# Optimization experiments

Hardware: AMD Instinct MI355X
Metric: run time of the kernel (lower is better)

Reference implementation:

```python
import jax, jax.numpy as jnp
import numpy as np

B, T, IN, H, OUT = 4096, 7, 512, 1024, 512


def setup_inputs() -> dict:
    key = jax.random.key(0)
    ks = jax.random.split(key, 13)
    s = 0.05  # weight init scale to keep gates/tanh unsaturated
    return {
        "x": jax.random.normal(ks[0], (B, T, IN), jnp.float32),
        "W_ih1": jax.random.normal(ks[1], (3 * H, IN), jnp.float32) * s,
        "W_hh1": jax.random.normal(ks[2], (3 * H, H), jnp.float32) * s,
        "b_ih1": jax.random.normal(ks[3], (3 * H,), jnp.float32) * s,
        "b_hh1": jax.random.normal(ks[4], (3 * H,), jnp.float32) * s,
        "W_ih2": jax.random.normal(ks[5], (3 * H, H), jnp.float32) * s,
        "W_hh2": jax.random.normal(ks[6], (3 * H, H), jnp.float32) * s,
        "b_ih2": jax.random.normal(ks[7], (3 * H,), jnp.float32) * s,
        "b_hh2": jax.random.normal(ks[8], (3 * H,), jnp.float32) * s,
        "Wo1": jax.random.normal(ks[9], (OUT, H), jnp.float32) * s,
        "bo1": jax.random.normal(ks[10], (OUT,), jnp.float32) * s,
        "Wo2": jax.random.normal(ks[11], (OUT, H), jnp.float32) * s,
        "bo2": jax.random.normal(ks[12], (OUT,), jnp.float32) * s,
    }


def gru_cell(x, h, W_ih, W_hh, b_ih, b_hh):
    # torch.nn.GRUCell math, gate order (r, z, n)
    gi = x @ W_ih.T + b_ih          # [B, 3H]
    gh = h @ W_hh.T + b_hh          # [B, 3H]
    i_r, i_z, i_n = jnp.split(gi, 3, axis=-1)
    h_r, h_z, h_n = jnp.split(gh, 3, axis=-1)
    r = jax.nn.sigmoid(i_r + h_r)
    z = jax.nn.sigmoid(i_z + h_z)
    n = jnp.tanh(i_n + r * h_n)
    return (1.0 - z) * n + z * h


def reference(x, W_ih1, W_hh1, b_ih1, b_hh1, W_ih2, W_hh2, b_ih2, b_hh2,
              Wo1, bo1, Wo2, bo2):
    batch = x.shape[0]
    h1_0 = jnp.zeros((batch, H), x.dtype)
    h2_0 = jnp.zeros((batch, H), x.dtype)

    def step(carry, x_t):
        h1, h2 = carry
        h1 = gru_cell(x_t, h1, W_ih1, W_hh1, b_ih1, b_hh1)
        h2 = gru_cell(h1, h2, W_ih2, W_hh2, b_ih2, b_hh2)
        out = jnp.tanh(h1 @ Wo1.T + bo1) + jnp.tanh(h2 @ Wo2.T + bo2)
        # s_t_cached starts as T zeros and only T steps run, so the popped
        # cached state is always zeros: mse(h2, 0) == mean(h2**2)
        aux = jnp.mean(jnp.square(h2))
        return (h1, h2), (out, aux)

    xs = jnp.swapaxes(x, 0, 1)  # [T, B, IN]
    _, (outs, auxs) = jax.lax.scan(step, (h1_0, h2_0), xs)
    outputs = jnp.swapaxes(outs, 0, 1)  # [B, T, OUT]
    aux_loss = jnp.sum(auxs)
    return outputs, aux_loss
```

## Files before the change

kernel.cpp:

```cpp
#include <hip/hip_runtime.h>
#include <cstdint>

#define BB   4096
#define TT   7
#define INF  512
#define HH   1024
#define OUTF 512
#define G3   3072

typedef short bf16x8 __attribute__((ext_vector_type(8)));
typedef float f32x4  __attribute__((ext_vector_type(4)));

static __device__ __forceinline__ unsigned short f2bf(float f) {
  unsigned u = __float_as_uint(f);
  unsigned r = ((u >> 16) & 1u) + 0x7FFFu;
  return (unsigned short)((u + r) >> 16);
}
static __device__ __forceinline__ float bf2f(unsigned short s) {
  return __uint_as_float(((unsigned)s) << 16);
}

#define GLDS16(gp, lp)                                                        \
  __builtin_amdgcn_global_load_lds(                                           \
      (const __attribute__((address_space(1))) void*)(gp),                    \
      (__attribute__((address_space(3))) void*)(lp), 16, 0, 0)

__device__ __forceinline__ int xcd_swz(int bid, int nwg) {
  return (bid & 7) * (nwg >> 3) + (bid >> 3);
}

__global__ __launch_bounds__(256)
void cvt_f32_to_bf16_x4(const float* __restrict__ in, unsigned short* __restrict__ out, int n4) {
  int i = blockIdx.x * 256 + threadIdx.x;
  if (i >= n4) return;
  const float4 v = ((const float4*)in)[i];
  ushort4 o;
  o.x = f2bf(v.x); o.y = f2bf(v.y); o.z = f2bf(v.z); o.w = f2bf(v.w);
  ((ushort4*)out)[i] = o;
}

__global__ __launch_bounds__(256)
void cvt_x_transpose(const float* __restrict__ in, unsigned short* __restrict__ out) {
  const int i4 = blockIdx.x * 256 + threadIdx.x;
  const long e = (long)i4 << 2;
  const int i  = (int)(e & (INF - 1));
  const long bt = e >> 9;
  const int t = (int)(bt % TT), b = (int)(bt / TT);
  const float4 v = *(const float4*)(in + e);
  ushort4 o;
  o.x = f2bf(v.x); o.y = f2bf(v.y); o.z = f2bf(v.z); o.w = f2bf(v.w);
  *(ushort4*)(out + ((size_t)t * BB + b) * INF + i) = o;
}

template<int BM, int BN, int WM, int WN, int GN>
__device__ __forceinline__ void gemm_core(
    const unsigned short* __restrict__ A, long lda, long bm,
    const unsigned short* __restrict__ Wp, long ldw, int K,
    const float* __restrict__ biasp,
    void* __restrict__ Cp, long ldc,
    const float* __restrict__ addp, long ldadd, int mode)
{
  constexpr int ABUF = BM * 64;
  constexpr int WBUF = BN * 64;
  constexpr int AR = (BM * 8) / 256;
  constexpr int WR = (BN * 8) / 256;
  __shared__ __attribute__((aligned(16))) unsigned short sm[2 * (ABUF + WBUF)];
  unsigned short* As = sm;
  unsigned short* Ws = sm + 2 * ABUF;
  __attribute__((address_space(3))) unsigned short* lAs =
      (__attribute__((address_space(3))) unsigned short*)As;
  __attribute__((address_space(3))) unsigned short* lWs =
      (__attribute__((address_space(3))) unsigned short*)Ws;

  const int tid  = threadIdx.x;
  const int lane = tid & 63;
  const int wid  = tid >> 6;
  const int wr = (wid / GN) * (WM * 16);
  const int wc = (wid % GN) * (WN * 16);
  const int fr = lane & 15;
  const int q2 = lane >> 4;

  const unsigned short* gpa[AR];
  const unsigned short* gpw[WR];
  int lofa[AR], lofw[WR];
#pragma unroll
  for (int r = 0; r < AR; ++r) {
    const int id = r * 256 + tid;
    const int row = id >> 3, cc = id & 7;
    gpa[r] = A + (bm + row) * lda + (cc ^ (row & 7)) * 8;
    lofa[r] = id * 8;
  }
#pragma unroll
  for (int r = 0; r < WR; ++r) {
    const int id = r * 256 + tid;
    const int row = id >> 3, cc = id & 7;
    gpw[r] = Wp + (long)row * ldw + (cc ^ (row & 7)) * 8;
    lofw[r] = id * 8;
  }

#define STAGE(buf, kt) do {                                                   \
    _Pragma("unroll")                                                         \
    for (int r = 0; r < AR; ++r) GLDS16(gpa[r] + (kt), lAs + (buf) * ABUF + lofa[r]); \
    _Pragma("unroll")                                                         \
    for (int r = 0; r < WR; ++r) GLDS16(gpw[r] + (kt), lWs + (buf) * WBUF + lofw[r]); \
  } while (0)

  f32x4 acc[WM][WN] = {};
  STAGE(0, 0);
  __syncthreads();
  const int NK = K >> 6;
  for (int it = 0; it < NK; ++it) {
    const int cur = it & 1;
    if (it + 1 < NK) STAGE(cur ^ 1, (it + 1) << 6);
#pragma unroll
    for (int ks = 0; ks < 2; ++ks) {
      bf16x8 af[WM], wf[WN];
#pragma unroll
      for (int i = 0; i < WM; ++i) {
        const int row = wr + i * 16 + fr;
        const int ch  = (ks * 4 + q2) ^ (row & 7);
        af[i] = *(const bf16x8*)&As[cur * ABUF + row * 64 + ch * 8];
      }
#pragma unroll
      for (int i = 0; i < WN; ++i) {
        const int row = wc + i * 16 + fr;
        const int ch  = (ks * 4 + q2) ^ (row & 7);
        wf[i] = *(const bf16x8*)&Ws[cur * WBUF + row * 64 + ch * 8];
      }
#pragma unroll
      for (int mi = 0; mi < WM; ++mi)
#pragma unroll
        for (int ni = 0; ni < WN; ++ni)
          acc[mi][ni] = __builtin_amdgcn_mfma_f32_16x16x32_bf16(af[mi], wf[ni], acc[mi][ni], 0, 0, 0);
    }
    __syncthreads();
  }
#undef STAGE

  const int q = lane >> 4;
#pragma unroll
  for (int ni = 0; ni < WN; ++ni) {
    const int col = wc + ni * 16 + fr;
    const float bv = biasp[col];
#pragma unroll
    for (int mi = 0; mi < WM; ++mi) {
      const long row = bm + wr + mi * 16 + q * 4;
#pragma unroll
      for (int j = 0; j < 4; ++j) {
        const float v = acc[mi][ni][j] + bv;
        if (mode == 0)      ((float*)Cp)[(row + j) * ldc + col] = v;
        else if (mode == 1) ((float*)Cp)[(row + j) * ldc + col] = tanhf(v);
        else if (mode == 2) ((float*)Cp)[(row + j) * ldc + col] = tanhf(v) + addp[(row + j) * ldadd + col];
        else                ((unsigned short*)Cp)[(row + j) * ldc + col] = f2bf(v);
      }
    }
  }
}

__global__ __launch_bounds__(256)
void k_gi1(const unsigned short* __restrict__ A,
           const unsigned short* __restrict__ W, const float* __restrict__ bias,
           unsigned short* __restrict__ C, int gx)
{
  const int wg = xcd_swz(blockIdx.x, gridDim.x);
  const int bx = wg % gx, by = wg / gx;
  gemm_core<128,128,4,4,2>(A, INF, (long)bx * 128, W + (long)by * 128 * INF,
                           INF, INF, bias + by * 128, C + by * 128, G3, nullptr, 0, 3);
}

__global__ __launch_bounds__(256)
void k_gh_dual(const unsigned short* __restrict__ h1b, const unsigned short* __restrict__ h2b,
               const unsigned short* __restrict__ W1, const unsigned short* __restrict__ W2,
               const float* __restrict__ b1, const float* __restrict__ b2,
               unsigned short* __restrict__ gh1, unsigned short* __restrict__ gh2)
{
  const int wg = xcd_swz(blockIdx.x, gridDim.x);
  const int bx = wg % 32;
  const int by = (wg / 32) % 24;
  const int z  = wg / (32 * 24);
  const unsigned short* Aa = z ? h2b : h1b;
  const unsigned short* Ww = (z ? W2 : W1) + (long)by * 128 * HH;
  const float* bias = (z ? b2 : b1) + by * 128;
  unsigned short* C = (z ? gh2 : gh1) + by * 128;
  gemm_core<128,128,4,4,2>(Aa, HH, (long)bx * 128, Ww, HH, HH, bias, C, G3, nullptr, 0, 3);
}

__global__ __launch_bounds__(256)
void k_gi2_o1(const unsigned short* __restrict__ h1b,
              const unsigned short* __restrict__ Wih2, const float* __restrict__ bih2,
              unsigned short* __restrict__ gi2,
              const unsigned short* __restrict__ Wo1, const float* __restrict__ bo1,
              float* __restrict__ o1t)
{
  const int wg = xcd_swz(blockIdx.x, gridDim.x);
  const int bx = wg % 32;
  const int by = wg / 32;
  const bool g = (by < 24);
  const int bo = by - 24;
  const unsigned short* Ww = g ? (Wih2 + (long)by * 128 * HH) : (Wo1 + (long)bo * 128 * HH);
  const float* bias        = g ? (bih2 + by * 128)            : (bo1 + bo * 128);
  void* C                  = g ? (void*)(gi2 + by * 128)      : (void*)(o1t + bo * 128);
  const long ldc           = g ? (long)G3 : (long)OUTF;
  gemm_core<128,128,4,4,2>(h1b, HH, (long)bx * 128, Ww, HH, HH, bias, C, ldc,
                           nullptr, 0, g ? 3 : 1);
}

__global__ __launch_bounds__(256)
void k_o2_out(const unsigned short* __restrict__ h2b,
              const unsigned short* __restrict__ Wo2, const float* __restrict__ bo2,
              const float* __restrict__ o1t, float* __restrict__ outp)
{
  const int wg = xcd_swz(blockIdx.x, gridDim.x);
  const int bx = wg % 64;
  const int by = wg / 64;
  gemm_core<64,64,2,2,2>(h2b, HH, (long)bx * 64, Wo2 + (long)by * 64 * HH, HH, HH,
                         bo2 + by * 64, outp + by * 64, (long)TT * OUTF,
                         o1t + by * 64, OUTF, 2);
}

__global__ __launch_bounds__(256)
void k_gate(const unsigned short* __restrict__ gi, long gistride,
            const unsigned short* __restrict__ gh,
            unsigned short* __restrict__ hb,
            float* __restrict__ auxp)
{
  const int i4 = blockIdx.x * 256 + threadIdx.x;
  const int e  = i4 << 2;
  const int b = e >> 10;
  const int c = e & 1023;
  const unsigned short* g = gi + (long)b * gistride + c;
  const ushort4 a0 = *(const ushort4*)(g);
  const ushort4 a1 = *(const ushort4*)(g + HH);
  const ushort4 a2 = *(const ushort4*)(g + 2 * HH);
  const unsigned short* gg = gh + (long)b * G3 + c;
  const ushort4 b0 = *(const ushort4*)(gg);
  const ushort4 b1 = *(const ushort4*)(gg + HH);
  const ushort4 b2 = *(const ushort4*)(gg + 2 * HH);
  const f32x4 ir  = f32x4{bf2f(a0.x), bf2f(a0.y), bf2f(a0.z), bf2f(a0.w)};
  const f32x4 iz  = f32x4{bf2f(a1.x), bf2f(a1.y), bf2f(a1.z), bf2f(a1.w)};
  const f32x4 inn = f32x4{bf2f(a2.x), bf2f(a2.y), bf2f(a2.z), bf2f(a2.w)};
  const f32x4 hr  = f32x4{bf2f(b0.x), bf2f(b0.y), bf2f(b0.z), bf2f(b0.w)};
  const f32x4 hz  = f32x4{bf2f(b1.x), bf2f(b1.y), bf2f(b1.z), bf2f(b1.w)};
  const f32x4 hn  = f32x4{bf2f(b2.x), bf2f(b2.y), bf2f(b2.z), bf2f(b2.w)};
  const ushort4 ho = *(const ushort4*)(hb + e);
  const f32x4 h = f32x4{bf2f(ho.x), bf2f(ho.y), bf2f(ho.z), bf2f(ho.w)};
  f32x4 hnew;
  float vsum = 0.f;
#pragma unroll
  for (int j = 0; j < 4; ++j) {
    const float r = 1.f / (1.f + __expf(-(ir[j] + hr[j])));
    const float z = 1.f / (1.f + __expf(-(iz[j] + hz[j])));
    const float n = tanhf(inn[j] + r * hn[j]);
    hnew[j] = (1.f - z) * n + z * h[j];
    vsum += hnew[j] * hnew[j];
  }
  ushort4 o;
  o.x = f2bf(hnew[0]); o.y = f2bf(hnew[1]); o.z = f2bf(hnew[2]); o.w = f2bf(hnew[3]);
  *(ushort4*)(hb + e) = o;
  if (auxp != nullptr) {
#pragma unroll
    for (int off = 32; off > 0; off >>= 1) vsum += __shfl_down(vsum, off);
    __shared__ float wsum[4];
    if ((threadIdx.x & 63) == 0) wsum[threadIdx.x >> 6] = vsum;
    __syncthreads();
    if (threadIdx.x == 0) auxp[blockIdx.x] = wsum[0] + wsum[1] + wsum[2] + wsum[3];
  }
}

__global__ __launch_bounds__(256)
void aux_reduce(const float* __restrict__ p, int n, float* __restrict__ out, float scale) {
  float s = 0.f;
  for (int i = threadIdx.x; i < n; i += 256) s += p[i];
#pragma unroll
  for (int off = 32; off > 0; off >>= 1) s += __shfl_down(s, off);
  __shared__ float wsum[4];
  if ((threadIdx.x & 63) == 0) wsum[threadIdx.x >> 6] = s;
  __syncthreads();
  if (threadIdx.x == 0) out[0] = (wsum[0] + wsum[1] + wsum[2] + wsum[3]) * scale;
}

extern "C" void kernel_launch(void* const* d_in, const int* in_sizes, int n_in,
                              void* d_out, int out_size, void* d_ws, size_t ws_size,
                              hipStream_t stream) {
  const float* x    = (const float*)d_in[0];
  const float* Wih1 = (const float*)d_in[1];
  const float* Whh1 = (const float*)d_in[2];
  const float* bih1 = (const float*)d_in[3];
  const float* bhh1 = (const float*)d_in[4];
  const float* Wih2 = (const float*)d_in[5];
  const float* Whh2 = (const float*)d_in[6];
  const float* bih2 = (const float*)d_in[7];
  const float* bhh2 = (const float*)d_in[8];
  const float* Wo1  = (const float*)d_in[9];
  const float* bo1  = (const float*)d_in[10];
  const float* Wo2  = (const float*)d_in[11];
  const float* bo2  = (const float*)d_in[12];

  char* ws = (char*)d_ws;
  size_t off = 0;
  auto alloc = [&](size_t bytes) {
    char* p = ws + off;
    off = (off + bytes + 255) & ~(size_t)255;
    return p;
  };

  unsigned short* xbT   = (unsigned short*)alloc((size_t)BB * TT * INF * 2);
  unsigned short* wih1b = (unsigned short*)alloc((size_t)G3 * INF * 2);
  unsigned short* whh1b = (unsigned short*)alloc((size_t)G3 * HH * 2);
  unsigned short* wih2b = (unsigned short*)alloc((size_t)G3 * HH * 2);
  unsigned short* whh2b = (unsigned short*)alloc((size_t)G3 * HH * 2);
  unsigned short* wo1b  = (unsigned short*)alloc((size_t)OUTF * HH * 2);
  unsigned short* wo2b  = (unsigned short*)alloc((size_t)OUTF * HH * 2);
  unsigned short* h1b = (unsigned short*)alloc((size_t)BB * HH * 2);
  unsigned short* h2b = (unsigned short*)alloc((size_t)BB * HH * 2);
  unsigned short* gh1 = (unsigned short*)alloc((size_t)BB * G3 * 2);
  unsigned short* gh2 = (unsigned short*)alloc((size_t)BB * G3 * 2);
  float* o1t  = (float*)alloc((size_t)BB * OUTF * 4);
  float* auxp = (float*)alloc((size_t)TT * (BB * HH / 1024) * 4);
  unsigned short* gi2 = gh1;

  const size_t slab = (size_t)BB * G3 * 2;
  int Th = (int)((ws_size > off ? (ws_size - off) : 0) / (slab + 256));
  if (Th < 1) Th = 1;
  if (Th > TT) Th = TT;
  unsigned short* gi1s = (unsigned short*)alloc((size_t)Th * slab);

  float* aux = (float*)d_out + (size_t)BB * TT * OUTF;

  auto cvt = [&](const float* src, unsigned short* dst, size_t n) {
    int n4 = (int)(n / 4);
    cvt_f32_to_bf16_x4<<<dim3((n4 + 255) / 256), dim3(256), 0, stream>>>(src, dst, n4);
  };
  cvt_x_transpose<<<dim3(BB * TT * INF / 1024), dim3(256), 0, stream>>>(x, xbT);
  cvt(Wih1, wih1b, (size_t)G3 * INF);
  cvt(Whh1, whh1b, (size_t)G3 * HH);
  cvt(Wih2, wih2b, (size_t)G3 * HH);
  cvt(Whh2, whh2b, (size_t)G3 * HH);
  cvt(Wo1,  wo1b,  (size_t)OUTF * HH);
  cvt(Wo2,  wo2b,  (size_t)OUTF * HH);

  hipMemsetAsync(h1b, 0, (size_t)BB * HH * 2, stream);
  hipMemsetAsync(h2b, 0, (size_t)BB * HH * 2, stream);

  const dim3 blk(256);
  const int gateGrid = BB * HH / 1024;

  k_gi1<<<dim3(Th * 768), blk, 0, stream>>>(xbT, wih1b, bih1, gi1s, Th * 32);

  for (int t = 0; t < TT; ++t) {
    const unsigned short* gi1_t;
    if (t < Th) {
      gi1_t = gi1s + (size_t)t * slab / 2;
    } else {
      k_gi1<<<dim3(768), blk, 0, stream>>>(xbT + (size_t)t * BB * INF,
                                           wih1b, bih1, gi1s, 32);
      gi1_t = gi1s;
    }
    k_gh_dual<<<dim3(1536), blk, 0, stream>>>(h1b, h2b, whh1b, whh2b, bhh1, bhh2, gh1, gh2);
    k_gate<<<dim3(gateGrid), blk, 0, stream>>>(gi1_t, (long)G3, gh1, h1b, nullptr);
    k_gi2_o1<<<dim3(896), blk, 0, stream>>>(h1b, wih2b, bih2, gi2, wo1b, bo1, o1t);
    k_gate<<<dim3(gateGrid), blk, 0, stream>>>(gi2, (long)G3, gh2, h2b,
                                               auxp + (size_t)t * gateGrid);
    k_o2_out<<<dim3(512), blk, 0, stream>>>(h2b, wo2b, bo2, o1t,
                                            (float*)d_out + (size_t)t * OUTF);
  }
  aux_reduce<<<dim3(1), blk, 0, stream>>>(auxp, TT * gateGrid, aux,
                                          1.f / ((float)BB * (float)HH));
}
```

Baseline: 1.391 ms.

## Defer Wo2 output GEMM into next step's gi2/o1 launch with double-buffered o1

The per-step output projection for layer 2 (h2 @ Wo2 + tanh add) is moved out of its own launch and folded into the next step's combined gi2/Wo1 kernel as extra tile rows, reading the previous h2 before it is overwritten. o1 results are double-buffered so the previous step's o1 is still available, and a final standalone kernel handles the last step. This removes one launch per step and raises the Wo2 GEMM to 128x128 tiles. k_gi1 also reorders its block index so the gate dimension varies fastest. The risk is ordering: h2b must still hold the previous step's state when the fused kernel runs.

```diff
diff --git a/kernel.cpp b/kernel.cpp
--- a/kernel.cpp
+++ b/kernel.cpp
@@ -160,10 +160,10 @@
 __global__ __launch_bounds__(256)
 void k_gi1(const unsigned short* __restrict__ A,
            const unsigned short* __restrict__ W, const float* __restrict__ bias,
-           unsigned short* __restrict__ C, int gx)
+           unsigned short* __restrict__ C)
 {
   const int wg = xcd_swz(blockIdx.x, gridDim.x);
-  const int bx = wg % gx, by = wg / gx;
+  const int by = wg % 24, bx = wg / 24;
   gemm_core<128,128,4,4,2>(A, INF, (long)bx * 128, W + (long)by * 128 * INF,
                            INF, INF, bias + by * 128, C + by * 128, G3, nullptr, 0, 3);
 }
@@ -190,32 +190,46 @@
               const unsigned short* __restrict__ Wih2, const float* __restrict__ bih2,
               unsigned short* __restrict__ gi2,
               const unsigned short* __restrict__ Wo1, const float* __restrict__ bo1,
-              float* __restrict__ o1t)
+              float* __restrict__ o1t_cur,
+              const unsigned short* __restrict__ h2b,
+              const unsigned short* __restrict__ Wo2, const float* __restrict__ bo2,
+              const float* __restrict__ o1t_prev, float* __restrict__ out_prev)
 {
   const int wg = xcd_swz(blockIdx.x, gridDim.x);
   const int bx = wg % 32;
   const int by = wg / 32;
-  const bool g = (by < 24);
-  const int bo = by - 24;
-  const unsigned short* Ww = g ? (Wih2 + (long)by * 128 * HH) : (Wo1 + (long)bo * 128 * HH);
-  const float* bias        = g ? (bih2 + by * 128)            : (bo1 + bo * 128);
-  void* C                  = g ? (void*)(gi2 + by * 128)      : (void*)(o1t + bo * 128);
-  const long ldc           = g ? (long)G3 : (long)OUTF;
-  gemm_core<128,128,4,4,2>(h1b, HH, (long)bx * 128, Ww, HH, HH, bias, C, ldc,
-                           nullptr, 0, g ? 3 : 1);
-}
-
-__global__ __launch_bounds__(256)
-void k_o2_out(const unsigned short* __restrict__ h2b,
-              const unsigned short* __restrict__ Wo2, const float* __restrict__ bo2,
-              const float* __restrict__ o1t, float* __restrict__ outp)
+  const unsigned short* A = h1b;
+  const unsigned short* Ww; const float* bias; void* C; long ldc; int mode;
+  const float* addp = nullptr; long ldadd = 0;
+  if (by < 24) {
+    Ww = Wih2 + (long)by * 128 * HH; bias = bih2 + by * 128;
+    C = gi2 + by * 128; ldc = G3; mode = 3;
+  } else if (by < 28) {
+    const int bo = by - 24;
+    Ww = Wo1 + (long)bo * 128 * HH; bias = bo1 + bo * 128;
+    C = o1t_cur + bo * 128; ldc = OUTF; mode = 1;
+  } else {
+    const int bo = by - 28;
+    A = h2b;
+    Ww = Wo2 + (long)bo * 128 * HH; bias = bo2 + bo * 128;
+    C = out_prev + bo * 128; ldc = (long)TT * OUTF; mode = 2;
+    addp = o1t_prev + bo * 128; ldadd = OUTF;
+  }
+  gemm_core<128,128,4,4,2>(A, HH, (long)bx * 128, Ww, HH, HH, bias, C, ldc,
+                           addp, ldadd, mode);
+}
+
+__global__ __launch_bounds__(256)
+void k_o2f(const unsigned short* __restrict__ h2b,
+           const unsigned short* __restrict__ Wo2, const float* __restrict__ bo2,
+           const float* __restrict__ o1t, float* __restrict__ outp)
 {
   const int wg = xcd_swz(blockIdx.x, gridDim.x);
-  const int bx = wg % 64;
-  const int by = wg / 64;
-  gemm_core<64,64,2,2,2>(h2b, HH, (long)bx * 64, Wo2 + (long)by * 64 * HH, HH, HH,
-                         bo2 + by * 64, outp + by * 64, (long)TT * OUTF,
-                         o1t + by * 64, OUTF, 2);
+  const int bx = wg & 31;
+  const int by = wg >> 5;
+  gemm_core<128,128,4,4,2>(h2b, HH, (long)bx * 128, Wo2 + (long)by * 128 * HH, HH, HH,
+                           bo2 + by * 128, outp + by * 128, (long)TT * OUTF,
+                           o1t + by * 128, OUTF, 2);
 }
 
 __global__ __launch_bounds__(256)
@@ -315,9 +329,11 @@
   unsigned short* h2b = (unsigned short*)alloc((size_t)BB * HH * 2);
   unsigned short* gh1 = (unsigned short*)alloc((size_t)BB * G3 * 2);
   unsigned short* gh2 = (unsigned short*)alloc((size_t)BB * G3 * 2);
-  float* o1t  = (float*)alloc((size_t)BB * OUTF * 4);
+  float* o1t0 = (float*)alloc((size_t)BB * OUTF * 4);
+  float* o1t1 = (float*)alloc((size_t)BB * OUTF * 4);
   float* auxp = (float*)alloc((size_t)TT * (BB * HH / 1024) * 4);
   unsigned short* gi2 = gh1;
+  float* o1t[2] = { o1t0, o1t1 };
 
   const size_t slab = (size_t)BB * G3 * 2;
   int Th = (int)((ws_size > off ? (ws_size - off) : 0) / (slab + 256));
@@ -345,25 +361,28 @@
   const dim3 blk(256);
   const int gateGrid = BB * HH / 1024;
 
-  k_gi1<<<dim3(Th * 768), blk, 0, stream>>>(xbT, wih1b, bih1, gi1s, Th * 32);
+  k_gi1<<<dim3(Th * 768), blk, 0, stream>>>(xbT, wih1b, bih1, gi1s);
 
   for (int t = 0; t < TT; ++t) {
     const unsigned short* gi1_t;
     if (t < Th) {
-      gi1_t = gi1s + (size_t)t * slab / 2;
+      gi1_t = gi1s + (size_t)t * BB * G3;
     } else {
       k_gi1<<<dim3(768), blk, 0, stream>>>(xbT + (size_t)t * BB * INF,
-                                           wih1b, bih1, gi1s, 32);
+                                           wih1b, bih1, gi1s);
       gi1_t = gi1s;
     }
     k_gh_dual<<<dim3(1536), blk, 0, stream>>>(h1b, h2b, whh1b, whh2b, bhh1, bhh2, gh1, gh2);
     k_gate<<<dim3(gateGrid), blk, 0, stream>>>(gi1_t, (long)G3, gh1, h1b, nullptr);
-    k_gi2_o1<<<dim3(896), blk, 0, stream>>>(h1b, wih2b, bih2, gi2, wo1b, bo1, o1t);
+    k_gi2_o1<<<dim3(t ? 1024 : 896), blk, 0, stream>>>(
+        h1b, wih2b, bih2, gi2, wo1b, bo1, o1t[t & 1],
+        h2b, wo2b, bo2, o1t[(t + 1) & 1],
+        (float*)d_out + (size_t)(t > 0 ? t - 1 : 0) * OUTF);
     k_gate<<<dim3(gateGrid), blk, 0, stream>>>(gi2, (long)G3, gh2, h2b,
                                                auxp + (size_t)t * gateGrid);
-    k_o2_out<<<dim3(512), blk, 0, stream>>>(h2b, wo2b, bo2, o1t,
-                                            (float*)d_out + (size_t)t * OUTF);
-  }
+  }
+  k_o2f<<<dim3(128), blk, 0, stream>>>(h2b, wo2b, bo2, o1t[(TT - 1) & 1],
+                                       (float*)d_out + (size_t)(TT - 1) * OUTF);
   aux_reduce<<<dim3(1), blk, 0, stream>>>(auxp, TT * gateGrid, aux,
                                           1.f / ((float)BB * (float)HH));
 }
```

Measured after the change: 1.668 ms. 1.2x slower.
